# Kernel tuning notes

Hardware: AMD Instinct MI355X
Metric: run time of the kernel (lower is better)

Reference implementation:

```python
import jax, jax.numpy as jnp
import numpy as np

NUM_LAYER = 5
EMB_DIM = 128
N_NODES = 50000
N_EDGES = 600000
BN_EPS = 1e-5


def setup_inputs() -> dict:
    key = jax.random.key(0)
    ks = jax.random.split(key, 16)
    d, L = EMB_DIM, NUM_LAYER
    s = 0.05
    inp = {
        "x": jax.random.randint(ks[0], (N_NODES, 3), 0, 3),
        "edge_index": jax.random.randint(ks[1], (2, N_EDGES), 0, N_NODES),
        "edge_attr": jax.random.randint(ks[2], (N_EDGES, 2), 0, 4),
        # node-feature embedding tables
        "atom_emb": jax.random.normal(ks[3], (120, d)) * s,
        "chir_emb": jax.random.normal(ks[4], (3, d)) * s,
        "hyb_emb": jax.random.normal(ks[5], (7, d)) * s,
        # per-layer GIN params, stacked over layers
        "e1": jax.random.normal(ks[6], (L, 6, d)) * s,   # bond-type edge emb
        "e2": jax.random.normal(ks[7], (L, 4, d)) * s,   # bond-direction edge emb
        "W1": jax.random.normal(ks[8], (L, d, 2 * d)) * s,
        "b1": jnp.zeros((L, 2 * d)),
        "W2": jax.random.normal(ks[9], (L, 2 * d, d)) * s,
        "b2": jnp.zeros((L, d)),
        "gamma": jnp.ones((L, d)),
        "beta": jnp.zeros((L, d)),
    }
    return inp


def _gnn_forward(x, edge_index, edge_attr, atom_emb, chir_emb, hyb_emb,
                 e1, e2, W1, b1, W2, b2, gamma, beta):
    src, dst = edge_index[0], edge_index[1]
    # input node embedding: sum of three categorical embeddings -> [N, d]
    h = atom_emb[x[:, 0]] + chir_emb[x[:, 1]] + hyb_emb[x[:, 2]]
    for l in range(NUM_LAYER):
        # per-edge embedding fused from two categorical tables -> [E, d]
        ee = e1[l][edge_attr[:, 0]] + e2[l][edge_attr[:, 1]]
        # gather source features, add edge emb, scatter-add to destination
        msg = h[src] + ee                                  # [E, d]
        agg = jax.ops.segment_sum(msg, dst, num_segments=N_NODES)  # [N, d]
        # GIN MLP: Linear(d,2d) -> ReLU -> Linear(2d,d)
        h2 = jax.nn.relu(agg @ W1[l] + b1[l]) @ W2[l] + b2[l]
        # BatchNorm1d (training-mode batch statistics, biased var)
        mu = h2.mean(axis=0)
        var = h2.var(axis=0)
        h2 = gamma[l] * (h2 - mu) * jax.lax.rsqrt(var + BN_EPS) + beta[l]
        # ReLU on all but the last layer (dropout is identity in eval)
        h = h2 if l == NUM_LAYER - 1 else jax.nn.relu(h2)
    return h


def reference(x, edge_index, edge_attr, atom_emb, chir_emb, hyb_emb,
              e1, e2, W1, b1, W2, b2, gamma, beta):
    return _gnn_forward(x, edge_index, edge_attr, atom_emb, chir_emb, hyb_emb,
                        e1, e2, W1, b1, W2, b2, gamma, beta)
```

## Files before the change

### kernel.cpp

```cpp
#include <hip/hip_runtime.h>
#include <hip/hip_bf16.h>

#define NN 50000
#define NE 600000
#define D 128
#define NL 5
#define AGG_BLOCKS 2048
#define M_TILES 391
#define MLP_BLOCKS 256

typedef __hip_bfloat16 bf16;
typedef unsigned short ushort_t;
typedef _Float16 half_t;
typedef __attribute__((ext_vector_type(8))) _Float16 half8;
typedef __attribute__((ext_vector_type(4))) _Float16 half4;
typedef __attribute__((ext_vector_type(8))) short short8;
typedef __attribute__((ext_vector_type(4))) float f32x4;
typedef __attribute__((ext_vector_type(2))) float f32x2;

__device__ __forceinline__ float b2f(bf16 v) { return __bfloat162float(v); }

__device__ __forceinline__ float loadF(const void* p, long long i, int isf32) {
    if (isf32) return ((const float*)p)[i];
    return b2f(((const bf16*)p)[i]);
}

__global__ void detect_k(const void* __restrict__ atom, int* __restrict__ flag) {
    __shared__ int vote;
    if (threadIdx.x == 0) vote = 0;
    __syncthreads();
    unsigned short u = ((const unsigned short*)atom)[threadIdx.x];
    unsigned short ex = (u >> 7) & 0xFF;
    if (ex >= 0x90) atomicOr(&vote, 1);
    __syncthreads();
    if (threadIdx.x == 0) *flag = vote;
}

__global__ void zero_f(float* __restrict__ p, int n) {
    int i = blockIdx.x * 256 + threadIdx.x;
    if (i < n) p[i] = 0.f;
}
__global__ void zero_i(int* __restrict__ p, int n) {
    int i = blockIdx.x * 256 + threadIdx.x;
    if (i < n) p[i] = 0;
}

__global__ void prepw_k(const void* __restrict__ W1, const void* __restrict__ W2,
                        const void* __restrict__ e1, const void* __restrict__ e2,
                        const int* __restrict__ fl,
                        half_t* __restrict__ w1t, half_t* __restrict__ w2t,
                        float* __restrict__ combT) {
    int isf32 = *fl;
    int idx = blockIdx.x * 256 + threadIdx.x;
    const int per = NL * 2 * D * D;
    if (idx < per) {
        int l = idx / (2 * D * D);
        int r = idx % (2 * D * D);
        int n = r >> 7, k = r & 127;
        w1t[idx] = (half_t)loadF(W1, (long long)l * 2 * D * D + (long long)k * 256 + n, isf32);
    } else if (idx < 2 * per) {
        int j = idx - per;
        int l = j / (2 * D * D);
        int r = j % (2 * D * D);
        int n = r >> 8, k = r & 255;
        w2t[j] = (half_t)loadF(W2, (long long)l * 2 * D * D + (long long)k * D + n, isf32);
    } else if (idx < 2 * per + NL * 24 * D) {
        int j = idx - 2 * per;
        int l = j / (24 * D);
        int r = j % (24 * D);
        int c = r >> 7, f = r & 127;
        combT[j] = loadF(e1, (long long)l * 6 * D + (long long)(c >> 2) * D + f, isf32) +
                   loadF(e2, (long long)l * 4 * D + (long long)(c & 3) * D + f, isf32);
    }
}

__global__ void hist_k(const int* __restrict__ ei, int* __restrict__ deg) {
    int e = blockIdx.x * 256 + threadIdx.x;
    if (e < NE) atomicAdd(&deg[ei[NE + e]], 1);
}

__global__ void scan1_k(const int* __restrict__ deg, int* __restrict__ tmp,
                        int* __restrict__ partial) {
    __shared__ int s[256];
    int t = threadIdx.x;
    int i = blockIdx.x * 256 + t;
    int v = (i < NN) ? deg[i] : 0;
    s[t] = v;
    __syncthreads();
    for (int off = 1; off < 256; off <<= 1) {
        int x = (t >= off) ? s[t - off] : 0;
        __syncthreads();
        s[t] += x;
        __syncthreads();
    }
    if (i < NN) tmp[i] = s[t];
    if (t == 255) partial[blockIdx.x] = s[255];
}

__global__ void scan2_k(int* __restrict__ partial, int nb) {
    __shared__ int s[256];
    int t = threadIdx.x;
    int v = (t < nb) ? partial[t] : 0;
    s[t] = v;
    __syncthreads();
    for (int off = 1; off < 256; off <<= 1) {
        int x = (t >= off) ? s[t - off] : 0;
        __syncthreads();
        s[t] += x;
        __syncthreads();
    }
    int excl = s[t] - v;
    __syncthreads();
    if (t < nb) partial[t] = excl;
}

__global__ void scan3_k(const int* __restrict__ tmp, const int* __restrict__ partial,
                        const int* __restrict__ deg,
                        int* __restrict__ row_start, int* __restrict__ next) {
    int i = blockIdx.x * 256 + threadIdx.x;
    if (i >= NN) return;
    int incl = tmp[i] + partial[i >> 8];
    row_start[i + 1] = incl;
    next[i] = incl - deg[i];
    if (i == 0) row_start[0] = 0;
}

__global__ void fill_k(const int* __restrict__ ei, const int* __restrict__ ea,
                       int* __restrict__ next, int* __restrict__ csr) {
    int e = blockIdx.x * 256 + threadIdx.x;
    if (e >= NE) return;
    int src = ei[e];
    int dst = ei[NE + e];
    int c = ea[2 * e] * 4 + ea[2 * e + 1];
    int pos = atomicAdd(&next[dst], 1);
    csr[pos] = src | (c << 16);
}

__global__ void embed_k(const int* __restrict__ x,
                        const void* __restrict__ atom,
                        const void* __restrict__ chir,
                        const void* __restrict__ hyb,
                        const int* __restrict__ fl,
                        half_t* __restrict__ h2) {
    int isf32 = *fl;
    int idx = blockIdx.x * 256 + threadIdx.x;
    if (idx >= NN * 64) return;
    int n = idx >> 6, fp = (idx & 63) * 2;
    long long i0 = (long long)x[n * 3 + 0] * D + fp;
    long long i1 = (long long)x[n * 3 + 1] * D + fp;
    long long i2 = (long long)x[n * 3 + 2] * D + fp;
    float v0 = loadF(atom, i0, isf32) + loadF(chir, i1, isf32) + loadF(hyb, i2, isf32);
    float v1 = loadF(atom, i0 + 1, isf32) + loadF(chir, i1 + 1, isf32) + loadF(hyb, i2 + 1, isf32);
    half_t* dst = h2 + (long long)n * D + fp;
    dst[0] = (half_t)v0;
    dst[1] = (half_t)v1;
}

__global__ void norm_k(half_t* __restrict__ h2,
                       const float* __restrict__ stats,
                       const void* __restrict__ gm, const void* __restrict__ bt,
                       const int* __restrict__ fl, int lprev) {
    __shared__ float norm_s[2 * D];
    int isf32 = *fl;
    int tid = threadIdx.x;
    if (tid < D) {
        float mu = stats[tid] * (1.f / NN);
        float var = fmaxf(stats[D + tid] * (1.f / NN) - mu * mu, 0.f);
        float rs = rsqrtf(var + 1e-5f);
        float sc = rs * loadF(gm, (long long)lprev * D + tid, isf32);
        float sh = loadF(bt, (long long)lprev * D + tid, isf32) - mu * sc;
        norm_s[tid] = sc;
        norm_s[D + tid] = sh;
    }
    __syncthreads();
    int idx = blockIdx.x * 256 + tid;
    if (idx >= NN * 16) return;
    int fp = (idx & 15) * 8;
    half_t* p = h2 + (long long)(idx >> 4) * D + fp;
    half8 v = *(half8*)p;
#pragma unroll
    for (int j = 0; j < 8; ++j) {
        float f = fmaxf(fmaf((float)v[j], norm_s[fp + j], norm_s[D + fp + j]), 0.f);
        v[j] = (half_t)f;
    }
    *(half8*)p = v;
}

__global__ __launch_bounds__(256) void aggr_k(
        const half_t* __restrict__ h,
        const int* __restrict__ row_start,
        const int* __restrict__ csr,
        const float* __restrict__ combT, int layer,
        half_t* __restrict__ agg) {
    __shared__ float comb[24 * D];
    int tid = threadIdx.x;
    const float* ct = combT + layer * 24 * D;
    for (int i = tid * 4; i < 24 * D; i += 1024)
        *(f32x4*)&comb[i] = *(const f32x4*)(ct + i);
    __syncthreads();
    int lane = tid & 63;
    int qw = lane >> 4;
    int f8 = (lane & 15) * 8;
    int wgid = blockIdx.x * 4 + (tid >> 6);
    int n0 = (int)(((long long)wgid * NN) >> 13);
    int n1 = (int)(((long long)(wgid + 1) * NN) >> 13);
    int beg = row_start[n0];
    for (int n = n0; n < n1; ++n) {
        int end = row_start[n + 1];
        float a0[8], a1[8];
#pragma unroll
        for (int j = 0; j < 8; ++j) { a0[j] = 0.f; a1[j] = 0.f; }
        int i = beg;
        for (; i + 7 < end; i += 8) {
            int pk0 = csr[i + qw];
            int pk1 = csr[i + 4 + qw];
            half8 g0 = *(const half8*)(h + (long long)(pk0 & 0xFFFF) * D + f8);
            half8 g1 = *(const half8*)(h + (long long)(pk1 & 0xFFFF) * D + f8);
            const float* c0 = &comb[(pk0 >> 16) * D + f8];
            const float* c1 = &comb[(pk1 >> 16) * D + f8];
#pragma unroll
            for (int j = 0; j < 8; ++j) {
                a0[j] += (float)g0[j] + c0[j];
                a1[j] += (float)g1[j] + c1[j];
            }
        }
        for (; i + 3 < end; i += 4) {
            int pk = csr[i + qw];
            half8 g = *(const half8*)(h + (long long)(pk & 0xFFFF) * D + f8);
            const float* c = &comb[(pk >> 16) * D + f8];
#pragma unroll
            for (int j = 0; j < 8; ++j)
                a0[j] += (float)g[j] + c[j];
        }
        if (i + qw < end) {
            int pk = csr[i + qw];
            half8 g = *(const half8*)(h + (long long)(pk & 0xFFFF) * D + f8);
            const float* c = &comb[(pk >> 16) * D + f8];
#pragma unroll
            for (int j = 0; j < 8; ++j)
                a0[j] += (float)g[j] + c[j];
        }
        half8 o;
#pragma unroll
        for (int j = 0; j < 8; ++j) {
            float v = a0[j] + a1[j];
            v += __shfl_down(v, 32, 64);
            v += __shfl_down(v, 16, 64);
            o[j] = (half_t)v;
        }
        if (qw == 0)
            *(half8*)(agg + (long long)n * D + f8) = o;
        beg = end;
    }
}

__global__ __launch_bounds__(512) void mlp_k(
        const half_t* __restrict__ agg,
        const half_t* __restrict__ w1t, const half_t* __restrict__ w2t,
        const void* __restrict__ b1, const void* __restrict__ b2,
        const int* __restrict__ fl, int layer,
        half_t* __restrict__ h2,
        float* __restrict__ statsAdd, float* __restrict__ statsZero) {
    __shared__ ushort_t Bs1[256 * 136];
    __shared__ ushort_t Bs2[128 * 264];
    __shared__ ushort_t Ms[128 * 72];
    int isf32 = *fl;
    int tid = threadIdx.x;
    if (blockIdx.x == 0 && tid < 2 * D) statsZero[tid] = 0.f;

    const half_t* w1p = w1t + (long long)layer * 256 * 128;
    const half_t* w2p = w2t + (long long)layer * 128 * 256;
    for (int i = tid; i < 256 * 8; i += 512) {
        int r = i >> 3, kq = (i & 7) * 16;
        const ushort_t* src = (const ushort_t*)w1p + r * 128 + kq;
        ushort_t* dst = &Bs1[r * 136 + kq];
        *(short8*)dst = *(const short8*)src;
        *(short8*)(dst + 8) = *(const short8*)(src + 8);
    }
    for (int i = tid; i < 128 * 16; i += 512) {
        int r = i >> 4, kq = (i & 15) * 16;
        const ushort_t* src = (const ushort_t*)w2p + r * 256 + kq;
        ushort_t* dst = &Bs2[r * 264 + kq];
        *(short8*)dst = *(const short8*)src;
        *(short8*)(dst + 8) = *(const short8*)(src + 8);
    }
    __syncthreads();

    int w = tid >> 6, lane = tid & 63;
    int quad = lane >> 4, l16 = lane & 15;
    long long b1off = (long long)layer * 2 * D;
    long long b2off = (long long)layer * D;

    float ssum[8], sq[8];
#pragma unroll
    for (int t = 0; t < 8; ++t) { ssum[t] = 0.f; sq[t] = 0.f; }

    for (int tile = blockIdx.x; tile < M_TILES; tile += MLP_BLOCKS) {
        int m0 = tile * 128;
        int arow = m0 + w * 16 + l16;
        if (arow >= NN) arow = NN - 1;
        const half_t* ap = agg + (long long)arow * D + quad * 8;
        half8 afrag[4];
#pragma unroll
        for (int kk4 = 0; kk4 < 4; ++kk4)
            afrag[kk4] = *(const half8*)(ap + kk4 * 32);

        f32x4 acc[8];
#pragma unroll
        for (int t = 0; t < 8; ++t) acc[t] = (f32x4){0.f, 0.f, 0.f, 0.f};

#pragma unroll
        for (int nc = 0; nc < 4; ++nc) {
            f32x4 macc[4];
#pragma unroll
            for (int nt = 0; nt < 4; ++nt) macc[nt] = (f32x4){0.f, 0.f, 0.f, 0.f};
#pragma unroll
            for (int kk4 = 0; kk4 < 4; ++kk4) {
                half8 a = afrag[kk4];
#pragma unroll
                for (int nt = 0; nt < 4; ++nt) {
                    half8 b = *(const half8*)&Bs1[(nc * 64 + nt * 16 + l16) * 136 + kk4 * 32 + quad * 8];
                    macc[nt] = __builtin_amdgcn_mfma_f32_16x16x32_f16(a, b, macc[nt], 0, 0, 0);
                }
            }
#pragma unroll
            for (int nt = 0; nt < 4; ++nt) {
                float bias = loadF(b1, b1off + nc * 64 + nt * 16 + l16, isf32);
#pragma unroll
                for (int r = 0; r < 4; ++r) {
                    float v = fmaxf(macc[nt][r] + bias, 0.f);
                    half_t hv = (half_t)v;
                    Ms[(w * 16 + quad * 4 + r) * 72 + nt * 16 + l16] = *(ushort_t*)&hv;
                }
            }
            asm volatile("s_waitcnt lgkmcnt(0)" ::: "memory");
#pragma unroll
            for (int kk4 = 0; kk4 < 2; ++kk4) {
                half8 a = *(const half8*)&Ms[(w * 16 + l16) * 72 + kk4 * 32 + quad * 8];
#pragma unroll
                for (int t = 0; t < 8; ++t) {
                    half8 b = *(const half8*)&Bs2[((t >> 2) * 64 + (t & 3) * 16 + l16) * 264 + nc * 64 + kk4 * 32 + quad * 8];
                    acc[t] = __builtin_amdgcn_mfma_f32_16x16x32_f16(a, b, acc[t], 0, 0, 0);
                }
            }
        }
#pragma unroll
        for (int t = 0; t < 8; ++t) {
            int col = (t >> 2) * 64 + (t & 3) * 16 + l16;
            float bias = loadF(b2, b2off + col, isf32);
#pragma unroll
            for (int r = 0; r < 4; ++r) {
                int row = m0 + w * 16 + quad * 4 + r;
                if (row < NN) {
                    float v = acc[t][r] + bias;
                    h2[(long long)row * D + col] = (half_t)v;
                    ssum[t] += v; sq[t] += v * v;
                }
            }
        }
    }

#pragma unroll
    for (int t = 0; t < 8; ++t) {
        ssum[t] += __shfl_xor(ssum[t], 16, 64);
        ssum[t] += __shfl_xor(ssum[t], 32, 64);
        sq[t]   += __shfl_xor(sq[t], 16, 64);
        sq[t]   += __shfl_xor(sq[t], 32, 64);
    }
    __syncthreads();
    float* SSf = (float*)Ms;
    if (tid < 2 * D) SSf[tid] = 0.f;
    __syncthreads();
    if (quad == 0) {
#pragma unroll
        for (int t = 0; t < 8; ++t) {
            int col = (t >> 2) * 64 + (t & 3) * 16 + l16;
            atomicAdd(&SSf[col], ssum[t]);
            atomicAdd(&SSf[D + col], sq[t]);
        }
    }
    __syncthreads();
    if (tid < 2 * D) atomicAdd(&statsAdd[tid], SSf[tid]);
}

__global__ void apply_k(const half_t* __restrict__ h2,
                        const float* __restrict__ statsPrev,
                        const void* __restrict__ gm, const void* __restrict__ bt,
                        const int* __restrict__ fl,
                        float* __restrict__ out) {
    __shared__ float norm_s[2 * D];
    int isf32 = *fl;
    int tid = threadIdx.x;
    if (tid < D) {
        float mu = statsPrev[tid] * (1.f / NN);
        float var = fmaxf(statsPrev[D + tid] * (1.f / NN) - mu * mu, 0.f);
        float rs = rsqrtf(var + 1e-5f);
        float sc = rs * loadF(gm, (long long)(NL - 1) * D + tid, isf32);
        float sh = loadF(bt, (long long)(NL - 1) * D + tid, isf32) - mu * sc;
        norm_s[tid] = sc;
        norm_s[D + tid] = sh;
    }
    __syncthreads();
    int idx = blockIdx.x * 256 + tid;
    if (idx >= NN * 64) return;
    int fp = (idx & 63) * 2;
    unsigned hv = *(const unsigned*)(h2 + (long long)(idx >> 6) * D + fp);
    float v0 = fmaf((float)((const half_t*)&hv)[0], norm_s[fp], norm_s[D + fp]);
    float v1 = fmaf((float)((const half_t*)&hv)[1], norm_s[fp + 1], norm_s[D + fp + 1]);
    f32x2 o; o.x = v0; o.y = v1;
    *(f32x2*)(out + (long long)(idx >> 6) * D + fp) = o;
}

extern "C" void kernel_launch(void* const* d_in, const int* in_sizes, int n_in,
                              void* d_out, int out_size, void* d_ws, size_t ws_size,
                              hipStream_t stream) {
    const int* x     = (const int*)d_in[0];
    const int* ei    = (const int*)d_in[1];
    const int* ea    = (const int*)d_in[2];
    const void* atom = d_in[3];
    const void* chir = d_in[4];
    const void* hyb  = d_in[5];
    const void* e1   = d_in[6];
    const void* e2   = d_in[7];
    const void* W1   = d_in[8];
    const void* b1   = d_in[9];
    const void* W2   = d_in[10];
    const void* b2   = d_in[11];
    const void* gm   = d_in[12];
    const void* bt   = d_in[13];

    const size_t ND = (size_t)NN * D;

    char* base = (char*)d_ws;
    float* SP0     = (float*)base;
    float* SP1     = (float*)(base + 1024);
    int*   flag    = (int*)(base + 2048);
    char*  p       = base + 4096;
    half_t* h2     = (half_t*)p;  p += ND * 2;
    half_t* w1t    = (half_t*)p;  p += (size_t)NL * 2 * D * D * 2;
    half_t* w2t    = (half_t*)p;  p += (size_t)NL * 2 * D * D * 2;
    float* combT   = (float*)p;   p += (size_t)NL * 24 * D * 4;
    int* csr       = (int*)p;     p += (size_t)NE * 4;
    int* row_start = (int*)p;     p += (size_t)(NN + 1) * 4 + 12;
    int* deg       = (int*)p;     p += (size_t)NN * 4;
    int* tmp       = (int*)p;     p += (size_t)NN * 4;
    int* next      = (int*)p;     p += (size_t)NN * 4;
    int* partial   = (int*)p;

    half_t* aggf = (half_t*)d_out;

    const int N2_BLOCKS = (NN * 64 + 255) / 256;
    const int NRM_BLOCKS = (NN * 16 + 255) / 256;
    const int E_BLOCKS  = (NE + 255) / 256;
    const int N_BLOCKS  = (NN + 255) / 256;
    const int PW_BLOCKS = (2 * NL * 2 * D * D + NL * 24 * D + 255) / 256;

    detect_k<<<1, 256, 0, stream>>>(atom, flag);
    prepw_k<<<PW_BLOCKS, 256, 0, stream>>>(W1, W2, e1, e2, flag, w1t, w2t, combT);

    zero_i<<<N_BLOCKS, 256, 0, stream>>>(deg, NN);
    hist_k<<<E_BLOCKS, 256, 0, stream>>>(ei, deg);
    scan1_k<<<N_BLOCKS, 256, 0, stream>>>(deg, tmp, partial);
    scan2_k<<<1, 256, 0, stream>>>(partial, N_BLOCKS);
    scan3_k<<<N_BLOCKS, 256, 0, stream>>>(tmp, partial, deg, row_start, next);
    fill_k<<<E_BLOCKS, 256, 0, stream>>>(ei, ea, next, csr);

    embed_k<<<N2_BLOCKS, 256, 0, stream>>>(x, atom, chir, hyb, flag, h2);
    zero_f<<<2, 256, 0, stream>>>(SP0, 2 * 2 * D);

    for (int l = 0; l < NL; ++l) {
        float* sPrev = ((l - 1) & 1) ? SP1 : SP0;
        float* sAdd  = (l & 1) ? SP1 : SP0;
        float* sZero = ((l + 1) & 1) ? SP1 : SP0;
        if (l > 0)
            norm_k<<<NRM_BLOCKS, 256, 0, stream>>>(h2, sPrev, gm, bt, flag, l - 1);
        aggr_k<<<AGG_BLOCKS, 256, 0, stream>>>(h2, row_start, csr, combT, l, aggf);
        mlp_k<<<MLP_BLOCKS, 512, 0, stream>>>(aggf, w1t, w2t, b1, b2, flag, l,
                                              h2, sAdd, sZero);
    }
    apply_k<<<N2_BLOCKS, 256, 0, stream>>>(h2, SP0, gm, bt, flag, (float*)d_out);
}
```

Baseline: 513.4 us.

## Fuse BatchNorm apply into MLP kernel via software grid barrier

Removes the separate per-layer norm kernel and the final apply kernel. mlp_k now increments a per-layer atomic counter after accumulating its BN statistics and spins until all blocks have arrived. It then computes scale and shift from the global stats and normalises h2 in place, applying ReLU for hidden layers or writing fp32 output for the last layer. This saves kernel launches and a separate pass, but depends on all 256 blocks being co-resident; with about 152 KB of LDS per block, that means one block per CU.

Result: slower. 580.1 us (+13.0%).

```diff
diff --git a/kernel.cpp b/kernel.cpp
--- a/kernel.cpp
+++ b/kernel.cpp
@@ -156,36 +156,6 @@
     dst[1] = (half_t)v1;
 }
 
-__global__ void norm_k(half_t* __restrict__ h2,
-                       const float* __restrict__ stats,
-                       const void* __restrict__ gm, const void* __restrict__ bt,
-                       const int* __restrict__ fl, int lprev) {
-    __shared__ float norm_s[2 * D];
-    int isf32 = *fl;
-    int tid = threadIdx.x;
-    if (tid < D) {
-        float mu = stats[tid] * (1.f / NN);
-        float var = fmaxf(stats[D + tid] * (1.f / NN) - mu * mu, 0.f);
-        float rs = rsqrtf(var + 1e-5f);
-        float sc = rs * loadF(gm, (long long)lprev * D + tid, isf32);
-        float sh = loadF(bt, (long long)lprev * D + tid, isf32) - mu * sc;
-        norm_s[tid] = sc;
-        norm_s[D + tid] = sh;
-    }
-    __syncthreads();
-    int idx = blockIdx.x * 256 + tid;
-    if (idx >= NN * 16) return;
-    int fp = (idx & 15) * 8;
-    half_t* p = h2 + (long long)(idx >> 4) * D + fp;
-    half8 v = *(half8*)p;
-#pragma unroll
-    for (int j = 0; j < 8; ++j) {
-        float f = fmaxf(fmaf((float)v[j], norm_s[fp + j], norm_s[D + fp + j]), 0.f);
-        v[j] = (half_t)f;
-    }
-    *(half8*)p = v;
-}
-
 __global__ __launch_bounds__(256) void aggr_k(
         const half_t* __restrict__ h,
         const int* __restrict__ row_start,
@@ -258,9 +228,11 @@
         const half_t* __restrict__ agg,
         const half_t* __restrict__ w1t, const half_t* __restrict__ w2t,
         const void* __restrict__ b1, const void* __restrict__ b2,
+        const void* __restrict__ gm, const void* __restrict__ bt,
         const int* __restrict__ fl, int layer,
         half_t* __restrict__ h2,
-        float* __restrict__ statsAdd, float* __restrict__ statsZero) {
+        float* __restrict__ statsAdd, float* __restrict__ statsZero,
+        int* __restrict__ cnt, float* __restrict__ out) {
     __shared__ ushort_t Bs1[256 * 136];
     __shared__ ushort_t Bs2[128 * 264];
     __shared__ ushort_t Ms[128 * 72];
@@ -381,34 +353,58 @@
     }
     __syncthreads();
     if (tid < 2 * D) atomicAdd(&statsAdd[tid], SSf[tid]);
-}
-
-__global__ void apply_k(const half_t* __restrict__ h2,
-                        const float* __restrict__ statsPrev,
-                        const void* __restrict__ gm, const void* __restrict__ bt,
-                        const int* __restrict__ fl,
-                        float* __restrict__ out) {
-    __shared__ float norm_s[2 * D];
-    int isf32 = *fl;
-    int tid = threadIdx.x;
+    __syncthreads();
+
+    if (tid == 0) {
+        __threadfence();
+        atomicAdd(&cnt[layer], 1);
+        while (atomicAdd(&cnt[layer], 0) < MLP_BLOCKS)
+            __builtin_amdgcn_s_sleep(2);
+    }
+    __syncthreads();
+
+    float* NS = (float*)Ms;
     if (tid < D) {
-        float mu = statsPrev[tid] * (1.f / NN);
-        float var = fmaxf(statsPrev[D + tid] * (1.f / NN) - mu * mu, 0.f);
+        float s = atomicAdd(&statsAdd[tid], 0.f);
+        float q = atomicAdd(&statsAdd[D + tid], 0.f);
+        float mu = s * (1.f / NN);
+        float var = fmaxf(q * (1.f / NN) - mu * mu, 0.f);
         float rs = rsqrtf(var + 1e-5f);
-        float sc = rs * loadF(gm, (long long)(NL - 1) * D + tid, isf32);
-        float sh = loadF(bt, (long long)(NL - 1) * D + tid, isf32) - mu * sc;
-        norm_s[tid] = sc;
-        norm_s[D + tid] = sh;
-    }
-    __syncthreads();
-    int idx = blockIdx.x * 256 + tid;
-    if (idx >= NN * 64) return;
-    int fp = (idx & 63) * 2;
-    unsigned hv = *(const unsigned*)(h2 + (long long)(idx >> 6) * D + fp);
-    float v0 = fmaf((float)((const half_t*)&hv)[0], norm_s[fp], norm_s[D + fp]);
-    float v1 = fmaf((float)((const half_t*)&hv)[1], norm_s[fp + 1], norm_s[D + fp + 1]);
-    f32x2 o; o.x = v0; o.y = v1;
-    *(f32x2*)(out + (long long)(idx >> 6) * D + fp) = o;
+        float sc = rs * loadF(gm, (long long)layer * D + tid, isf32);
+        float sh = loadF(bt, (long long)layer * D + tid, isf32) - mu * sc;
+        NS[tid] = sc;
+        NS[D + tid] = sh;
+    }
+    __syncthreads();
+    int lastL = (layer == NL - 1);
+    for (int tile = blockIdx.x; tile < M_TILES; tile += MLP_BLOCKS) {
+        int m0 = tile * 128;
+        for (int i2 = tid; i2 < 128 * 16; i2 += 512) {
+            int row = m0 + (i2 >> 4);
+            if (row >= NN) break;
+            int fp = (i2 & 15) * 8;
+            half_t* ph = h2 + (long long)row * D + fp;
+            half8 v = *(half8*)ph;
+            if (!lastL) {
+#pragma unroll
+                for (int j = 0; j < 8; ++j) {
+                    float f = fmaxf(fmaf((float)v[j], NS[fp + j], NS[D + fp + j]), 0.f);
+                    v[j] = (half_t)f;
+                }
+                *(half8*)ph = v;
+            } else {
+                f32x4 o0, o1;
+#pragma unroll
+                for (int j = 0; j < 4; ++j)
+                    o0[j] = fmaf((float)v[j], NS[fp + j], NS[D + fp + j]);
+#pragma unroll
+                for (int j = 0; j < 4; ++j)
+                    o1[j] = fmaf((float)v[4 + j], NS[fp + 4 + j], NS[D + fp + 4 + j]);
+                *(f32x4*)(out + (long long)row * D + fp) = o0;
+                *(f32x4*)(out + (long long)row * D + fp + 4) = o1;
+            }
+        }
+    }
 }
 
 extern "C" void kernel_launch(void* const* d_in, const int* in_sizes, int n_in,
@@ -435,6 +431,7 @@
     float* SP0     = (float*)base;
     float* SP1     = (float*)(base + 1024);
     int*   flag    = (int*)(base + 2048);
+    int*   cnt     = (int*)(base + 2304);
     char*  p       = base + 4096;
     half_t* h2     = (half_t*)p;  p += ND * 2;
     half_t* w1t    = (half_t*)p;  p += (size_t)NL * 2 * D * D * 2;
@@ -450,7 +447,6 @@
     half_t* aggf = (half_t*)d_out;
 
     const int N2_BLOCKS = (NN * 64 + 255) / 256;
-    const int NRM_BLOCKS = (NN * 16 + 255) / 256;
     const int E_BLOCKS  = (NE + 255) / 256;
     const int N_BLOCKS  = (NN + 255) / 256;
     const int PW_BLOCKS = (2 * NL * 2 * D * D + NL * 24 * D + 255) / 256;
@@ -467,16 +463,14 @@
 
     embed_k<<<N2_BLOCKS, 256, 0, stream>>>(x, atom, chir, hyb, flag, h2);
     zero_f<<<2, 256, 0, stream>>>(SP0, 2 * 2 * D);
+    zero_i<<<1, 64, 0, stream>>>(cnt, 8);
 
     for (int l = 0; l < NL; ++l) {
-        float* sPrev = ((l - 1) & 1) ? SP1 : SP0;
         float* sAdd  = (l & 1) ? SP1 : SP0;
         float* sZero = ((l + 1) & 1) ? SP1 : SP0;
-        if (l > 0)
-            norm_k<<<NRM_BLOCKS, 256, 0, stream>>>(h2, sPrev, gm, bt, flag, l - 1);
         aggr_k<<<AGG_BLOCKS, 256, 0, stream>>>(h2, row_start, csr, combT, l, aggf);
-        mlp_k<<<MLP_BLOCKS, 512, 0, stream>>>(aggf, w1t, w2t, b1, b2, flag, l,
-                                              h2, sAdd, sZero);
-    }
-    apply_k<<<N2_BLOCKS, 256, 0, stream>>>(h2, SP0, gm, bt, flag, (float*)d_out);
-}
+        mlp_k<<<MLP_BLOCKS, 512, 0, stream>>>(aggf, w1t, w2t, b1, b2, gm, bt,
+                                              flag, l, h2, sAdd, sZero, cnt,
+                                              (float*)d_out);
+    }
+}
```

## Read MLP weights directly from global memory and launch one block per tile

Applied to the files above, without the earlier changes.

The MLP kernel no longer stages W1 and W2 into shared memory. Each wave now loads its B fragments straight from global memory, relying on L1/L2 caching. The persistent tile loop is replaced by one 512-thread block per 128-row tile, with launch_bounds raised to allow 4 blocks per CU. This removes the per-block weight-staging prologue and the large LDS footprint so more blocks fit per CU. In exchange every wave re-reads the full weights from cache instead of LDS. The shared stats buffer is zeroed at kernel start with no barrier before the atomics that accumulate into it.

Measured after the change: 719.1 us. +40.1%, slower.

```diff
diff --git a/kernel.cpp b/kernel.cpp
--- a/kernel.cpp
+++ b/kernel.cpp
@@ -7,7 +7,6 @@
 #define NL 5
 #define AGG_BLOCKS 2048
 #define M_TILES 391
-#define MLP_BLOCKS 256
 
 typedef __hip_bfloat16 bf16;
 typedef unsigned short ushort_t;
@@ -254,112 +253,92 @@
     }
 }
 
-__global__ __launch_bounds__(512) void mlp_k(
+__global__ __launch_bounds__(512, 4) void mlp_k(
         const half_t* __restrict__ agg,
         const half_t* __restrict__ w1t, const half_t* __restrict__ w2t,
         const void* __restrict__ b1, const void* __restrict__ b2,
         const int* __restrict__ fl, int layer,
         half_t* __restrict__ h2,
         float* __restrict__ statsAdd, float* __restrict__ statsZero) {
-    __shared__ ushort_t Bs1[256 * 136];
-    __shared__ ushort_t Bs2[128 * 264];
     __shared__ ushort_t Ms[128 * 72];
+    __shared__ float SS[2 * D];
     int isf32 = *fl;
     int tid = threadIdx.x;
     if (blockIdx.x == 0 && tid < 2 * D) statsZero[tid] = 0.f;
-
-    const half_t* w1p = w1t + (long long)layer * 256 * 128;
-    const half_t* w2p = w2t + (long long)layer * 128 * 256;
-    for (int i = tid; i < 256 * 8; i += 512) {
-        int r = i >> 3, kq = (i & 7) * 16;
-        const ushort_t* src = (const ushort_t*)w1p + r * 128 + kq;
-        ushort_t* dst = &Bs1[r * 136 + kq];
-        *(short8*)dst = *(const short8*)src;
-        *(short8*)(dst + 8) = *(const short8*)(src + 8);
-    }
-    for (int i = tid; i < 128 * 16; i += 512) {
-        int r = i >> 4, kq = (i & 15) * 16;
-        const ushort_t* src = (const ushort_t*)w2p + r * 256 + kq;
-        ushort_t* dst = &Bs2[r * 264 + kq];
-        *(short8*)dst = *(const short8*)src;
-        *(short8*)(dst + 8) = *(const short8*)(src + 8);
-    }
-    __syncthreads();
-
+    if (tid < 2 * D) SS[tid] = 0.f;
     int w = tid >> 6, lane = tid & 63;
     int quad = lane >> 4, l16 = lane & 15;
     long long b1off = (long long)layer * 2 * D;
     long long b2off = (long long)layer * D;
+    int m0 = blockIdx.x * 128;
+
+    int arow = m0 + w * 16 + l16;
+    if (arow >= NN) arow = NN - 1;
+    const half_t* ap = agg + (long long)arow * D + quad * 8;
+    half8 afrag[4];
+#pragma unroll
+    for (int kk4 = 0; kk4 < 4; ++kk4)
+        afrag[kk4] = *(const half8*)(ap + kk4 * 32);
+
+    const half_t* w1p = w1t + (long long)layer * 256 * 128;
+    const half_t* w2p = w2t + (long long)layer * 128 * 256;
+    f32x4 acc[8];
+#pragma unroll
+    for (int t = 0; t < 8; ++t) acc[t] = (f32x4){0.f, 0.f, 0.f, 0.f};
+
+#pragma unroll
+    for (int nc = 0; nc < 4; ++nc) {
+        f32x4 macc[4];
+#pragma unroll
+        for (int nt = 0; nt < 4; ++nt) macc[nt] = (f32x4){0.f, 0.f, 0.f, 0.f};
+#pragma unroll
+        for (int kk4 = 0; kk4 < 4; ++kk4) {
+            half8 a = afrag[kk4];
+#pragma unroll
+            for (int nt = 0; nt < 4; ++nt) {
+                half8 b = *(const half8*)(w1p + (long long)(nc * 64 + nt * 16 + l16) * 128 + kk4 * 32 + quad * 8);
+                macc[nt] = __builtin_amdgcn_mfma_f32_16x16x32_f16(a, b, macc[nt], 0, 0, 0);
+            }
+        }
+#pragma unroll
+        for (int nt = 0; nt < 4; ++nt) {
+            float bias = loadF(b1, b1off + nc * 64 + nt * 16 + l16, isf32);
+#pragma unroll
+            for (int r = 0; r < 4; ++r) {
+                float v = fmaxf(macc[nt][r] + bias, 0.f);
+                half_t hv = (half_t)v;
+                Ms[(w * 16 + quad * 4 + r) * 72 + nt * 16 + l16] = *(ushort_t*)&hv;
+            }
+        }
+        asm volatile("s_waitcnt lgkmcnt(0)" ::: "memory");
+#pragma unroll
+        for (int kk4 = 0; kk4 < 2; ++kk4) {
+            half8 a = *(const half8*)&Ms[(w * 16 + l16) * 72 + kk4 * 32 + quad * 8];
+#pragma unroll
+            for (int t = 0; t < 8; ++t) {
+                half8 b = *(const half8*)(w2p + (long long)((t >> 2) * 64 + (t & 3) * 16 + l16) * 256 + nc * 64 + kk4 * 32 + quad * 8);
+                acc[t] = __builtin_amdgcn_mfma_f32_16x16x32_f16(a, b, acc[t], 0, 0, 0);
+            }
+        }
+    }
 
     float ssum[8], sq[8];
 #pragma unroll
     for (int t = 0; t < 8; ++t) { ssum[t] = 0.f; sq[t] = 0.f; }
-
-    for (int tile = blockIdx.x; tile < M_TILES; tile += MLP_BLOCKS) {
-        int m0 = tile * 128;
-        int arow = m0 + w * 16 + l16;
-        if (arow >= NN) arow = NN - 1;
-        const half_t* ap = agg + (long long)arow * D + quad * 8;
-        half8 afrag[4];
-#pragma unroll
-        for (int kk4 = 0; kk4 < 4; ++kk4)
-            afrag[kk4] = *(const half8*)(ap + kk4 * 32);
-
-        f32x4 acc[8];
-#pragma unroll
-        for (int t = 0; t < 8; ++t) acc[t] = (f32x4){0.f, 0.f, 0.f, 0.f};
-
-#pragma unroll
-        for (int nc = 0; nc < 4; ++nc) {
-            f32x4 macc[4];
-#pragma unroll
-            for (int nt = 0; nt < 4; ++nt) macc[nt] = (f32x4){0.f, 0.f, 0.f, 0.f};
-#pragma unroll
-            for (int kk4 = 0; kk4 < 4; ++kk4) {
-                half8 a = afrag[kk4];
-#pragma unroll
-                for (int nt = 0; nt < 4; ++nt) {
-                    half8 b = *(const half8*)&Bs1[(nc * 64 + nt * 16 + l16) * 136 + kk4 * 32 + quad * 8];
-                    macc[nt] = __builtin_amdgcn_mfma_f32_16x16x32_f16(a, b, macc[nt], 0, 0, 0);
-                }
+#pragma unroll
+    for (int t = 0; t < 8; ++t) {
+        int col = (t >> 2) * 64 + (t & 3) * 16 + l16;
+        float bias = loadF(b2, b2off + col, isf32);
+#pragma unroll
+        for (int r = 0; r < 4; ++r) {
+            int row = m0 + w * 16 + quad * 4 + r;
+            if (row < NN) {
+                float v = acc[t][r] + bias;
+                h2[(long long)row * D + col] = (half_t)v;
+                ssum[t] += v; sq[t] += v * v;
             }
-#pragma unroll
-            for (int nt = 0; nt < 4; ++nt) {
-                float bias = loadF(b1, b1off + nc * 64 + nt * 16 + l16, isf32);
-#pragma unroll
-                for (int r = 0; r < 4; ++r) {
-                    float v = fmaxf(macc[nt][r] + bias, 0.f);
-                    half_t hv = (half_t)v;
-                    Ms[(w * 16 + quad * 4 + r) * 72 + nt * 16 + l16] = *(ushort_t*)&hv;
-                }
-            }
-            asm volatile("s_waitcnt lgkmcnt(0)" ::: "memory");
-#pragma unroll
-            for (int kk4 = 0; kk4 < 2; ++kk4) {
-                half8 a = *(const half8*)&Ms[(w * 16 + l16) * 72 + kk4 * 32 + quad * 8];
-#pragma unroll
-                for (int t = 0; t < 8; ++t) {
-                    half8 b = *(const half8*)&Bs2[((t >> 2) * 64 + (t & 3) * 16 + l16) * 264 + nc * 64 + kk4 * 32 + quad * 8];
-                    acc[t] = __builtin_amdgcn_mfma_f32_16x16x32_f16(a, b, acc[t], 0, 0, 0);
-                }
-            }
-        }
-#pragma unroll
-        for (int t = 0; t < 8; ++t) {
-            int col = (t >> 2) * 64 + (t & 3) * 16 + l16;
-            float bias = loadF(b2, b2off + col, isf32);
-#pragma unroll
-            for (int r = 0; r < 4; ++r) {
-                int row = m0 + w * 16 + quad * 4 + r;
-                if (row < NN) {
-                    float v = acc[t][r] + bias;
-                    h2[(long long)row * D + col] = (half_t)v;
-                    ssum[t] += v; sq[t] += v * v;
-                }
-            }
-        }
-    }
-
+        }
+    }
 #pragma unroll
     for (int t = 0; t < 8; ++t) {
         ssum[t] += __shfl_xor(ssum[t], 16, 64);
@@ -367,20 +346,16 @@
         sq[t]   += __shfl_xor(sq[t], 16, 64);
         sq[t]   += __shfl_xor(sq[t], 32, 64);
     }
-    __syncthreads();
-    float* SSf = (float*)Ms;
-    if (tid < 2 * D) SSf[tid] = 0.f;
-    __syncthreads();
     if (quad == 0) {
 #pragma unroll
         for (int t = 0; t < 8; ++t) {
             int col = (t >> 2) * 64 + (t & 3) * 16 + l16;
-            atomicAdd(&SSf[col], ssum[t]);
-            atomicAdd(&SSf[D + col], sq[t]);
-        }
-    }
-    __syncthreads();
-    if (tid < 2 * D) atomicAdd(&statsAdd[tid], SSf[tid]);
+            atomicAdd(&SS[col], ssum[t]);
+            atomicAdd(&SS[D + col], sq[t]);
+        }
+    }
+    __syncthreads();
+    if (tid < 2 * D) atomicAdd(&statsAdd[tid], SS[tid]);
 }
 
 __global__ void apply_k(const half_t* __restrict__ h2,
@@ -475,8 +450,8 @@
         if (l > 0)
             norm_k<<<NRM_BLOCKS, 256, 0, stream>>>(h2, sPrev, gm, bt, flag, l - 1);
         aggr_k<<<AGG_BLOCKS, 256, 0, stream>>>(h2, row_start, csr, combT, l, aggf);
-        mlp_k<<<MLP_BLOCKS, 512, 0, stream>>>(aggf, w1t, w2t, b1, b2, flag, l,
-                                              h2, sAdd, sZero);
+        mlp_k<<<M_TILES, 512, 0, stream>>>(aggf, w1t, w2t, b1, b2, flag, l,
+                                           h2, sAdd, sZero);
     }
     apply_k<<<N2_BLOCKS, 256, 0, stream>>>(h2, SP0, gm, bt, flag, (float*)d_out);
 }
```
